# Kernel optimization log

Hardware: AMD Instinct MI355X
Metric: run time of the kernel (lower is better)

The kernel has to match this reference:

```python
import jax, jax.numpy as jnp
import numpy as np

N, H, G = 500_000, 128, 1024

def setup_inputs() -> dict:
    key = jax.random.key(0)
    k1, k2, k3, k4 = jax.random.split(key, 4)
    x = jax.random.normal(k1, (N, H), dtype=jnp.float32)
    batch = jnp.sort(jax.random.randint(k2, (N,), 0, G)).astype(jnp.int64)
    gate_w = jax.random.normal(k3, (H, 1), dtype=jnp.float32) * (1.0 / np.sqrt(H))
    gate_b = jnp.zeros((1,), dtype=jnp.float32)
    combine_w = jax.random.normal(k4, (3 * H, H), dtype=jnp.float32) * (1.0 / np.sqrt(3 * H))
    combine_b = jnp.zeros((H,), dtype=jnp.float32)
    return {"x": x, "batch": batch, "gate_w": gate_w, "gate_b": gate_b,
            "combine_w": combine_w, "combine_b": combine_b, "num_graphs": G}

def reference(x, batch, gate_w, gate_b, combine_w, combine_b, num_graphs):
    # --- GlobalAttention pool: segment softmax over gate scores, weighted sum ---
    gate = (x @ gate_w + gate_b)[:, 0]                                  # [N]
    gmax = jax.ops.segment_max(gate, batch, num_segments=num_graphs)    # [G]
    gmax = jnp.where(jnp.isfinite(gmax), gmax, 0.0)                     # guard empty segments
    e = jnp.exp(gate - gmax[batch])                                     # [N]
    denom = jax.ops.segment_sum(e, batch, num_segments=num_graphs)      # [G]
    alpha = e / jnp.maximum(denom, 1e-16)[batch]                        # [N]
    att = jax.ops.segment_sum(alpha[:, None] * x, batch, num_segments=num_graphs)  # [G,H]

    # --- global_mean_pool ---
    s = jax.ops.segment_sum(x, batch, num_segments=num_graphs)          # [G,H]
    cnt = jax.ops.segment_sum(jnp.ones((x.shape[0],), x.dtype), batch, num_segments=num_graphs)
    mean = s / jnp.maximum(cnt, 1.0)[:, None]

    # --- global_max_pool ---
    mx = jax.ops.segment_max(x, batch, num_segments=num_graphs)         # [G,H]
    mx = jnp.where(jnp.isfinite(mx), mx, 0.0)

    combined = jnp.concatenate([att, mean, mx], axis=1)                 # [G,3H]
    return combined @ combine_w + combine_b                             # [G,H]
```

## Files before the change

### kernel.cpp

```cpp
#include <hip/hip_runtime.h>
#include <math.h>

#define H 128

__global__ __launch_bounds__(256, 4)
void pool_kernel(const float* __restrict__ x,
                 const int* __restrict__ batch,
                 const float* __restrict__ gate_w,
                 const float* __restrict__ gate_b,
                 const float* __restrict__ combine_w,
                 const float* __restrict__ combine_b,
                 float* __restrict__ out,
                 int N)
{
    const int g    = blockIdx.x;
    const int t    = threadIdx.x;
    const int grp  = t >> 5;
    const int lane = t & 31;

    __shared__ int   s_range[2];
    __shared__ float s_att[8][H];
    __shared__ float s_sum[8][H];
    __shared__ float s_mx[8][H];
    __shared__ float s_m[8], s_d[8];
    __shared__ float s_comb[3 * H];
    __shared__ float s_part[H];

    if (t < 2) {
        int target = g + t;
        int lo = 0, hi = N;
        while (lo < hi) {
            int mid = (lo + hi) >> 1;
            if (batch[mid] < target) lo = mid + 1; else hi = mid;
        }
        s_range[t] = lo;
    }
    __syncthreads();
    const int start = s_range[0];
    const int end   = s_range[1];
    const int cnt   = end - start;

    const float4 gw = ((const float4*)gate_w)[lane];
    const float  gb = gate_b[0];

    float  m = -INFINITY, d = 0.0f;
    float4 att = make_float4(0.f, 0.f, 0.f, 0.f);
    float4 sum = make_float4(0.f, 0.f, 0.f, 0.f);
    float4 mx  = make_float4(-INFINITY, -INFINITY, -INFINITY, -INFINITY);

    const float4* xv = (const float4*)x;

    int   r    = start + grp;
    bool  curv = (r < end);
    float4 cur = make_float4(0.f, 0.f, 0.f, 0.f);
    if (curv) cur = xv[(size_t)r * 32 + lane];

    while (curv) {
        int    rn   = r + 8;
        bool   nxtv = (rn < end);
        float4 nxt  = make_float4(0.f, 0.f, 0.f, 0.f);
        if (nxtv) nxt = xv[(size_t)rn * 32 + lane];

        float p = cur.x * gw.x + cur.y * gw.y + cur.z * gw.z + cur.w * gw.w;
        p += __shfl_xor(p, 1);
        p += __shfl_xor(p, 2);
        p += __shfl_xor(p, 4);
        p += __shfl_xor(p, 8);
        p += __shfl_xor(p, 16);
        float gate = p + gb;

        float nm = fmaxf(m, gate);
        float sc = __expf(m - nm);
        float e  = __expf(gate - nm);
        m = nm;
        d = d * sc + e;
        att.x = att.x * sc + e * cur.x;
        att.y = att.y * sc + e * cur.y;
        att.z = att.z * sc + e * cur.z;
        att.w = att.w * sc + e * cur.w;

        sum.x += cur.x; sum.y += cur.y; sum.z += cur.z; sum.w += cur.w;
        mx.x = fmaxf(mx.x, cur.x);
        mx.y = fmaxf(mx.y, cur.y);
        mx.z = fmaxf(mx.z, cur.z);
        mx.w = fmaxf(mx.w, cur.w);

        r = rn; cur = nxt; curv = nxtv;
    }

    ((float4*)s_att[grp])[lane] = att;
    ((float4*)s_sum[grp])[lane] = sum;
    ((float4*)s_mx[grp])[lane]  = mx;
    if (lane == 0) { s_m[grp] = m; s_d[grp] = d; }
    __syncthreads();

    if (t < H) {
        const int f = t;
        float M = -INFINITY;
        #pragma unroll
        for (int k = 0; k < 8; k++) M = fmaxf(M, s_m[k]);

        float D = 0.f, attf = 0.f, sm = 0.f, mxf = -INFINITY;
        #pragma unroll
        for (int k = 0; k < 8; k++) {
            float w = __expf(s_m[k] - M);
            D    += w * s_d[k];
            attf += w * s_att[k][f];
            sm   += s_sum[k][f];
            mxf   = fmaxf(mxf, s_mx[k][f]);
        }

        float o_att, o_mean, o_mx;
        if (cnt > 0) {
            o_att  = attf / fmaxf(D, 1e-16f);
            o_mean = sm / (float)cnt;
            o_mx   = mxf;
        } else {
            o_att = 0.f; o_mean = 0.f; o_mx = 0.f;
        }
        s_comb[f]         = o_att;
        s_comb[H + f]     = o_mean;
        s_comb[2 * H + f] = o_mx;
    }
    __syncthreads();

    {
        const int j    = t & (H - 1);
        const int half = t >> 7;
        const int k0   = half * 192;
        float acc = 0.f;
        #pragma unroll 8
        for (int k = k0; k < k0 + 192; k++)
            acc += s_comb[k] * combine_w[k * H + j];
        if (half == 0) s_part[j] = acc;
        __syncthreads();
        if (half == 1)
            out[(size_t)g * H + j] = acc + s_part[j] + combine_b[j];
    }
}

extern "C" void kernel_launch(void* const* d_in, const int* in_sizes, int n_in,
                              void* d_out, int out_size, void* d_ws, size_t ws_size,
                              hipStream_t stream) {
    const float* x         = (const float*)d_in[0];
    const int*   batch     = (const int*)d_in[1];
    const float* gate_w    = (const float*)d_in[2];
    const float* gate_b    = (const float*)d_in[3];
    const float* combine_w = (const float*)d_in[4];
    const float* combine_b = (const float*)d_in[5];
    float* out = (float*)d_out;

    const int N = in_sizes[0] / H;
    const int G = out_size / H;

    pool_kernel<<<G, 256, 0, stream>>>(x, batch, gate_w, gate_b,
                                       combine_w, combine_b, out, N);
}
```

Measured before the change: 372.8 us.

## Split pooling into row-chunk accumulation with atomics plus a per-graph finish kernel

Result: slower. 381.8 us (+2.4%).

```diff
diff --git a/kernel.cpp b/kernel.cpp
--- a/kernel.cpp
+++ b/kernel.cpp
@@ -2,141 +2,195 @@
 #include <math.h>
 
 #define H 128
+#define CHUNK 256
+
+__device__ __forceinline__ unsigned fenc(float v) {
+    unsigned u = __float_as_uint(v);
+    return (u & 0x80000000u) ? ~u : (u | 0x80000000u);
+}
+__device__ __forceinline__ float fdec(unsigned u) {
+    return __uint_as_float((u & 0x80000000u) ? (u ^ 0x80000000u) : ~u);
+}
 
 __global__ __launch_bounds__(256, 4)
-void pool_kernel(const float* __restrict__ x,
-                 const int* __restrict__ batch,
-                 const float* __restrict__ gate_w,
-                 const float* __restrict__ gate_b,
-                 const float* __restrict__ combine_w,
-                 const float* __restrict__ combine_b,
-                 float* __restrict__ out,
-                 int N)
+void accum_kernel(const float* __restrict__ x,
+                  const int*   __restrict__ batch,
+                  const float* __restrict__ gate_w,
+                  const float* __restrict__ gate_b,
+                  float*    __restrict__ ws_att,
+                  float*    __restrict__ ws_sum,
+                  unsigned* __restrict__ ws_mx,
+                  float*    __restrict__ ws_den,
+                  unsigned* __restrict__ ws_cnt,
+                  int N)
 {
-    const int g    = blockIdx.x;
     const int t    = threadIdx.x;
     const int grp  = t >> 5;
     const int lane = t & 31;
-
-    __shared__ int   s_range[2];
+    const int r0   = blockIdx.x * CHUNK;
+    if (r0 >= N) return;
+    const int len  = min(CHUNK, N - r0);
+
+    __shared__ int s_b[CHUNK];
+    __shared__ unsigned long long s_mask[4];
     __shared__ float s_att[8][H];
     __shared__ float s_sum[8][H];
     __shared__ float s_mx[8][H];
-    __shared__ float s_m[8], s_d[8];
+    __shared__ float s_d[8];
+
+    if (t < len) s_b[t] = batch[r0 + t];
+    __syncthreads();
+    bool flag = (t > 0) && (t < len) && (s_b[t] != s_b[t - 1]);
+    unsigned long long bm = __ballot(flag);
+    if ((t & 63) == 0) s_mask[t >> 6] = bm;
+    __syncthreads();
+
+    const float4 gw = ((const float4*)gate_w)[lane];
+    const float  gb = gate_b[0];
+    const float4* xv = (const float4*)x;
+
+    int s = 0;
+    while (s < len) {
+        const int g = s_b[s];
+
+        int e = len;
+        {
+            int w = (s + 1) >> 6;
+            if (w < 4) {
+                unsigned long long mm = s_mask[w] & (~0ULL << ((s + 1) & 63));
+                while (true) {
+                    if (mm) { e = (w << 6) + __ffsll(mm) - 1; break; }
+                    if (++w >= 4) break;
+                    mm = s_mask[w];
+                }
+            }
+        }
+        const int aS = r0 + s, aE = r0 + e;
+
+        float  d   = 0.0f;
+        float4 att = make_float4(0.f, 0.f, 0.f, 0.f);
+        float4 sum = make_float4(0.f, 0.f, 0.f, 0.f);
+        float4 mx  = make_float4(-INFINITY, -INFINITY, -INFINITY, -INFINITY);
+
+        int  rA = aS + grp;
+        bool v0 = rA     < aE;
+        bool v1 = rA + 8 < aE;
+        float4 c0 = make_float4(0.f, 0.f, 0.f, 0.f);
+        float4 c1 = make_float4(0.f, 0.f, 0.f, 0.f);
+        if (v0) c0 = xv[(size_t)rA * 32 + lane];
+        if (v1) c1 = xv[(size_t)(rA + 8) * 32 + lane];
+
+        while (v0) {
+            const int rN = rA + 16;
+            bool n0v = rN     < aE;
+            bool n1v = rN + 8 < aE;
+            float4 n0 = make_float4(0.f, 0.f, 0.f, 0.f);
+            float4 n1 = make_float4(0.f, 0.f, 0.f, 0.f);
+            if (n0v) n0 = xv[(size_t)rN * 32 + lane];
+            if (n1v) n1 = xv[(size_t)(rN + 8) * 32 + lane];
+
+            float p0 = c0.x*gw.x + c0.y*gw.y + c0.z*gw.z + c0.w*gw.w;
+            float p1 = c1.x*gw.x + c1.y*gw.y + c1.z*gw.z + c1.w*gw.w;
+            p0 += __shfl_xor(p0, 1);  p1 += __shfl_xor(p1, 1);
+            p0 += __shfl_xor(p0, 2);  p1 += __shfl_xor(p1, 2);
+            p0 += __shfl_xor(p0, 4);  p1 += __shfl_xor(p1, 4);
+            p0 += __shfl_xor(p0, 8);  p1 += __shfl_xor(p1, 8);
+            p0 += __shfl_xor(p0, 16); p1 += __shfl_xor(p1, 16);
+
+            float e0 = __expf(p0 + gb);
+            float e1 = v1 ? __expf(p1 + gb) : 0.0f;
+
+            d += e0 + e1;
+            att.x += e0*c0.x + e1*c1.x;
+            att.y += e0*c0.y + e1*c1.y;
+            att.z += e0*c0.z + e1*c1.z;
+            att.w += e0*c0.w + e1*c1.w;
+            sum.x += c0.x + c1.x;
+            sum.y += c0.y + c1.y;
+            sum.z += c0.z + c1.z;
+            sum.w += c0.w + c1.w;
+            mx.x = fmaxf(mx.x, c0.x); mx.y = fmaxf(mx.y, c0.y);
+            mx.z = fmaxf(mx.z, c0.z); mx.w = fmaxf(mx.w, c0.w);
+            if (v1) {
+                mx.x = fmaxf(mx.x, c1.x); mx.y = fmaxf(mx.y, c1.y);
+                mx.z = fmaxf(mx.z, c1.z); mx.w = fmaxf(mx.w, c1.w);
+            }
+            rA = rN; c0 = n0; c1 = n1; v0 = n0v; v1 = n1v;
+        }
+
+        ((float4*)s_att[grp])[lane] = att;
+        ((float4*)s_sum[grp])[lane] = sum;
+        ((float4*)s_mx[grp])[lane]  = mx;
+        if (lane == 0) s_d[grp] = d;
+        __syncthreads();
+
+        if (t < H) {
+            float a = 0.f, sm = 0.f, mxf = -INFINITY;
+            #pragma unroll
+            for (int k = 0; k < 8; k++) {
+                a  += s_att[k][t];
+                sm += s_sum[k][t];
+                mxf = fmaxf(mxf, s_mx[k][t]);
+            }
+            atomicAdd(&ws_att[(size_t)g * H + t], a);
+            atomicAdd(&ws_sum[(size_t)g * H + t], sm);
+            atomicMax(&ws_mx[(size_t)g * H + t], fenc(mxf));
+        } else if (t == H) {
+            float D = 0.f;
+            #pragma unroll
+            for (int k = 0; k < 8; k++) D += s_d[k];
+            atomicAdd(&ws_den[g], D);
+            atomicAdd(&ws_cnt[g], (unsigned)(e - s));
+        }
+        __syncthreads();
+        s = e;
+    }
+}
+
+__global__ __launch_bounds__(256, 4)
+void finish_kernel(const float*    __restrict__ ws_att,
+                   const float*    __restrict__ ws_sum,
+                   const unsigned* __restrict__ ws_mx,
+                   const float*    __restrict__ ws_den,
+                   const unsigned* __restrict__ ws_cnt,
+                   const float*    __restrict__ combine_w,
+                   const float*    __restrict__ combine_b,
+                   float*          __restrict__ out)
+{
+    const int g = blockIdx.x;
+    const int t = threadIdx.x;
+
     __shared__ float s_comb[3 * H];
     __shared__ float s_part[H];
 
-    if (t < 2) {
-        int target = g + t;
-        int lo = 0, hi = N;
-        while (lo < hi) {
-            int mid = (lo + hi) >> 1;
-            if (batch[mid] < target) lo = mid + 1; else hi = mid;
-        }
-        s_range[t] = lo;
-    }
-    __syncthreads();
-    const int start = s_range[0];
-    const int end   = s_range[1];
-    const int cnt   = end - start;
-
-    const float4 gw = ((const float4*)gate_w)[lane];
-    const float  gb = gate_b[0];
-
-    float  m = -INFINITY, d = 0.0f;
-    float4 att = make_float4(0.f, 0.f, 0.f, 0.f);
-    float4 sum = make_float4(0.f, 0.f, 0.f, 0.f);
-    float4 mx  = make_float4(-INFINITY, -INFINITY, -INFINITY, -INFINITY);
-
-    const float4* xv = (const float4*)x;
-
-    int   r    = start + grp;
-    bool  curv = (r < end);
-    float4 cur = make_float4(0.f, 0.f, 0.f, 0.f);
-    if (curv) cur = xv[(size_t)r * 32 + lane];
-
-    while (curv) {
-        int    rn   = r + 8;
-        bool   nxtv = (rn < end);
-        float4 nxt  = make_float4(0.f, 0.f, 0.f, 0.f);
-        if (nxtv) nxt = xv[(size_t)rn * 32 + lane];
-
-        float p = cur.x * gw.x + cur.y * gw.y + cur.z * gw.z + cur.w * gw.w;
-        p += __shfl_xor(p, 1);
-        p += __shfl_xor(p, 2);
-        p += __shfl_xor(p, 4);
-        p += __shfl_xor(p, 8);
-        p += __shfl_xor(p, 16);
-        float gate = p + gb;
-
-        float nm = fmaxf(m, gate);
-        float sc = __expf(m - nm);
-        float e  = __expf(gate - nm);
-        m = nm;
-        d = d * sc + e;
-        att.x = att.x * sc + e * cur.x;
-        att.y = att.y * sc + e * cur.y;
-        att.z = att.z * sc + e * cur.z;
-        att.w = att.w * sc + e * cur.w;
-
-        sum.x += cur.x; sum.y += cur.y; sum.z += cur.z; sum.w += cur.w;
-        mx.x = fmaxf(mx.x, cur.x);
-        mx.y = fmaxf(mx.y, cur.y);
-        mx.z = fmaxf(mx.z, cur.z);
-        mx.w = fmaxf(mx.w, cur.w);
-
-        r = rn; cur = nxt; curv = nxtv;
-    }
-
-    ((float4*)s_att[grp])[lane] = att;
-    ((float4*)s_sum[grp])[lane] = sum;
-    ((float4*)s_mx[grp])[lane]  = mx;
-    if (lane == 0) { s_m[grp] = m; s_d[grp] = d; }
-    __syncthreads();
-
     if (t < H) {
-        const int f = t;
-        float M = -INFINITY;
-        #pragma unroll
-        for (int k = 0; k < 8; k++) M = fmaxf(M, s_m[k]);
-
-        float D = 0.f, attf = 0.f, sm = 0.f, mxf = -INFINITY;
-        #pragma unroll
-        for (int k = 0; k < 8; k++) {
-            float w = __expf(s_m[k] - M);
-            D    += w * s_d[k];
-            attf += w * s_att[k][f];
-            sm   += s_sum[k][f];
-            mxf   = fmaxf(mxf, s_mx[k][f]);
-        }
-
+        unsigned cnt = ws_cnt[g];
         float o_att, o_mean, o_mx;
         if (cnt > 0) {
-            o_att  = attf / fmaxf(D, 1e-16f);
-            o_mean = sm / (float)cnt;
-            o_mx   = mxf;
+            float D = ws_den[g];
+            o_att  = ws_att[(size_t)g * H + t] / fmaxf(D, 1e-16f);
+            o_mean = ws_sum[(size_t)g * H + t] / (float)cnt;
+            o_mx   = fdec(ws_mx[(size_t)g * H + t]);
         } else {
             o_att = 0.f; o_mean = 0.f; o_mx = 0.f;
         }
-        s_comb[f]         = o_att;
-        s_comb[H + f]     = o_mean;
-        s_comb[2 * H + f] = o_mx;
+        s_comb[t]         = o_att;
+        s_comb[H + t]     = o_mean;
+        s_comb[2 * H + t] = o_mx;
     }
     __syncthreads();
 
-    {
-        const int j    = t & (H - 1);
-        const int half = t >> 7;
-        const int k0   = half * 192;
-        float acc = 0.f;
-        #pragma unroll 8
-        for (int k = k0; k < k0 + 192; k++)
-            acc += s_comb[k] * combine_w[k * H + j];
-        if (half == 0) s_part[j] = acc;
-        __syncthreads();
-        if (half == 1)
-            out[(size_t)g * H + j] = acc + s_part[j] + combine_b[j];
-    }
+    const int j    = t & (H - 1);
+    const int half = t >> 7;
+    const int k0   = half * 192;
+    float acc = 0.f;
+    #pragma unroll 8
+    for (int k = k0; k < k0 + 192; k++)
+        acc += s_comb[k] * combine_w[k * H + j];
+    if (half == 0) s_part[j] = acc;
+    __syncthreads();
+    if (half == 1)
+        out[(size_t)g * H + j] = acc + s_part[j] + combine_b[j];
 }
 
 extern "C" void kernel_launch(void* const* d_in, const int* in_sizes, int n_in,
@@ -153,6 +207,18 @@
     const int N = in_sizes[0] / H;
     const int G = out_size / H;
 
-    pool_kernel<<<G, 256, 0, stream>>>(x, batch, gate_w, gate_b,
-                                       combine_w, combine_b, out, N);
-}
+    float*    ws_att = (float*)d_ws;
+    float*    ws_sum = ws_att + (size_t)G * H;
+    unsigned* ws_mx  = (unsigned*)(ws_sum + (size_t)G * H);
+    float*    ws_den = (float*)(ws_mx + (size_t)G * H);
+    unsigned* ws_cnt = (unsigned*)(ws_den + G);
+    const size_t ws_bytes = ((size_t)3 * G * H + 2 * (size_t)G) * sizeof(float);
+
+    hipMemsetAsync(d_ws, 0, ws_bytes, stream);
+
+    const int nblk = (N + CHUNK - 1) / CHUNK;
+    accum_kernel<<<nblk, 256, 0, stream>>>(x, batch, gate_w, gate_b,
+                                           ws_att, ws_sum, ws_mx, ws_den, ws_cnt, N);
+    finish_kernel<<<G, 256, 0, stream>>>(ws_att, ws_sum, ws_mx, ws_den, ws_cnt,
+                                         combine_w, combine_b, out);
+}
```
